# Optimization experiments

Measured on AMD Instinct MI355X. Metric: run time of the kernel, lower is better.

## Reference

```python
import jax, jax.numpy as jnp
import numpy as np

N, F, D, M, B, K = 100000, 256, 128, 10, 32768, 32


def setup_inputs() -> dict:
    key = jax.random.key(0)
    ks = jax.random.split(key, 14)
    stdv = float(1.0 / np.sqrt(D))
    inp = {
        "feature": jax.random.normal(ks[0], (N, F), jnp.float32),
        "flow_char_adj": jax.random.uniform(ks[1], (M, N), jnp.float32),
        "history": jax.random.randint(ks[2], (B, K), 0, N),
        "item_id": jax.random.randint(ks[3], (B,), 0, N),
        "category_r": jax.random.randint(ks[4], (B,), 0, 2),
        "category_n": jax.random.randint(ks[5], (B,), 0, 2),
        "PA_level": jax.random.randint(ks[6], (B,), 0, M),
        # learned parameters (uniform(-stdv, stdv) as in reset_parameters)
        "weight_emb": jax.random.uniform(ks[7], (F, D), jnp.float32, -stdv, stdv),
        "bias_emb": jax.random.uniform(ks[8], (D,), jnp.float32, -stdv, stdv),
        "weight_character": jax.random.uniform(ks[9], (2 * D, D), jnp.float32, -stdv, stdv),
        "att1_w": jax.random.uniform(ks[10], (D, 1), jnp.float32, -stdv, stdv),
        "att1_b": jax.random.uniform(ks[11], (1,), jnp.float32, -stdv, stdv),
        "linear1_w": jax.random.uniform(ks[12], (2 * D, D), jnp.float32, -stdv, stdv),
        "linear1_b": jax.random.uniform(ks[13], (D,), jnp.float32, -stdv, stdv),
    }
    return inp


def reference(feature, flow_char_adj, weight_emb, bias_emb, weight_character,
              att1_w, att1_b, linear1_w, linear1_b,
              history, item_id, category_r, category_n, PA_level):
    # embedding_encode
    flow_emb = feature @ weight_emb + bias_emb              # [N, D]
    character_emb = flow_char_adj @ flow_emb                # [M, D] (spmm)

    # character_modeling (shared for r and n)
    def char_lat(cat, pa):
        ce = jnp.concatenate([character_emb[cat], character_emb[pa]], axis=1)  # [B, 2D]
        return jax.nn.sigmoid(ce @ weight_character)        # [B, D]

    lat_r = char_lat(category_r, PA_level)
    lat_n = char_lat(category_n, PA_level)

    # attribute_agg: mix flow emb with its 2 category embeddings
    flow_all = (flow_emb + flow_char_adj[:2].T @ character_emb[:2]) * 0.5  # [N, D]

    # Flow_Aggregator: per-node neighbor attention (batched over ragged lists,
    # here padded to fixed degree K)
    neigh = flow_all[history]                                # [B, K, D]
    scores = neigh @ att1_w + att1_b                         # [B, K, 1]
    att = jax.nn.softmax(scores, axis=1)                     # softmax over neighbors
    agg = jnp.sum(att * neigh, axis=1)                       # [B, D]

    # NOTE: in the torch source, self_flow_latent is mutated in-place so
    # self_feats aliases neigh_feats -> both halves of the concat equal agg.
    combined = jnp.concatenate([agg, agg], axis=1)           # [B, 2D]
    out = jax.nn.relu(combined @ linear1_w + linear1_b)      # [B, D] (dropout p=0)

    pred_r = jnp.sum(lat_r * out, axis=1)                    # [B]
    pred_n = jnp.sum(lat_n * out, axis=1)                    # [B]
    return pred_r, pred_n
```

## Files before the change

### kernel.cpp

```cpp
#include <hip/hip_runtime.h>
#include <cmath>

#define NN 100000
#define FF 256
#define DDIM 128
#define MM 10
#define BB 32768
#define KK 32
#define NB1 782
#define NREP 64

#define OFF_Q     0
#define OFF_CEREP 100096
#define OFF_CE    182016
#define OFF_LAT   183296
#define OFF_CE01  185856
#define OFF_CS    186112
#define OFF_AGGB  186128
#define OFF_FE8   2283280
#define OFF_WF    5483280
#define OFF_WPF   5499664

typedef __attribute__((ext_vector_type(8))) short bf16x8;
typedef __attribute__((ext_vector_type(4))) float floatx4;
typedef __attribute__((ext_vector_type(2))) float floatx2;

__device__ __forceinline__ unsigned short f2bf(float x) {
  union { float f; unsigned u; } v; v.f = x;
  unsigned r = v.u + 0x7FFFu + ((v.u >> 16) & 1u);
  return (unsigned short)(r >> 16);
}

__device__ __forceinline__ bf16x8 cvt8(float4 a, float4 b) {
  short h[8];
  h[0] = (short)f2bf(a.x); h[1] = (short)f2bf(a.y);
  h[2] = (short)f2bf(a.z); h[3] = (short)f2bf(a.w);
  h[4] = (short)f2bf(b.x); h[5] = (short)f2bf(b.y);
  h[6] = (short)f2bf(b.z); h[7] = (short)f2bf(b.w);
  return *reinterpret_cast<bf16x8*>(h);
}

__global__ __launch_bounds__(256) void k0_wprep(const float* __restrict__ wemb,
                                                const float* __restrict__ l1w,
                                                short* __restrict__ wf,
                                                short* __restrict__ wpf)
{
  const int t = blockIdx.x * 256 + threadIdx.x;
  if (t < 4096) {
    const int kk = t >> 9, rem = t & 511;
    const int ct = rem >> 6, l = rem & 63;
    const int n = ct * 16 + (l & 15);
    const int kbase = kk * 32 + (l >> 4) * 8;
    short hi[8];
#pragma unroll
    for (int j = 0; j < 8; j++) hi[j] = (short)f2bf(wemb[(kbase + j) * 128 + n]);
    *reinterpret_cast<int4*>(&wf[((kk * 8 + ct) * 64 + l) * 8]) = *reinterpret_cast<int4*>(hi);
  } else {
    const int t2 = t - 4096;
    const int kk = t2 >> 9, rem = t2 & 511;
    const int ct = rem >> 6, l = rem & 63;
    const int n = ct * 16 + (l & 15);
    short h[8];
#pragma unroll
    for (int j = 0; j < 8; j++) {
      const int kp = kk * 32 + (l >> 4) * 8 + j;
      const int i = ((kp & 7) << 4) | (kp >> 3);
      h[j] = (short)f2bf(l1w[i * 128 + n] + l1w[(128 + i) * 128 + n]);
    }
    *reinterpret_cast<int4*>(&wpf[((kk * 8 + ct) * 64 + l) * 8]) = *reinterpret_cast<int4*>(h);
  }
}

__global__ __launch_bounds__(128, 2) void k1_fused(const float* __restrict__ feat,
    const short* __restrict__ wf, const float* __restrict__ bemb,
    const float* __restrict__ attw, const float* __restrict__ adj,
    float* __restrict__ q, unsigned char* __restrict__ fe8,
    float* __restrict__ cerep)
{
  __shared__ __align__(16) unsigned char ldst[128 * 272];
  const int tid = threadIdx.x;
  const int wv = tid >> 6, l = tid & 63;
  const int lane16 = l & 15, quad = l >> 4;

  floatx4 acc[4][8];
#pragma unroll
  for (int rt = 0; rt < 4; rt++)
#pragma unroll
    for (int ct = 0; ct < 8; ct++) acc[rt][ct] = floatx4{0.f, 0.f, 0.f, 0.f};

  const float* pa[4];
#pragma unroll
  for (int rt = 0; rt < 4; rt++) {
    int r = blockIdx.x * 128 + (wv * 4 + rt) * 16 + lane16;
    if (r > NN - 1) r = NN - 1;
    pa[rt] = &feat[(size_t)r * 256 + quad * 8];
  }

#pragma unroll 2
  for (int kk = 0; kk < 8; kk++) {
    const short* wb = &wf[kk * 4096 + l * 8];
    bf16x8 bh[8];
#pragma unroll
    for (int ct = 0; ct < 8; ct++)
      bh[ct] = *reinterpret_cast<const bf16x8*>(&wb[ct * 512]);
    bf16x8 a[4];
#pragma unroll
    for (int rt = 0; rt < 4; rt++) {
      const float4 f0 = *reinterpret_cast<const float4*>(pa[rt] + kk * 32);
      const float4 f1 = *reinterpret_cast<const float4*>(pa[rt] + kk * 32 + 4);
      a[rt] = cvt8(f0, f1);
    }
#pragma unroll
    for (int rt = 0; rt < 4; rt++)
#pragma unroll
      for (int ct = 0; ct < 8; ct++)
        acc[rt][ct] = __builtin_amdgcn_mfma_f32_16x16x32_bf16(a[rt], bh[ct], acc[rt][ct], 0, 0, 0);
  }

  float bembv[8], attwv[8];
#pragma unroll
  for (int ct = 0; ct < 8; ct++) {
    bembv[ct] = bemb[ct * 16 + lane16];
    attwv[ct] = attw[ct * 16 + lane16];
  }
#pragma unroll
  for (int rt = 0; rt < 4; rt++) {
#pragma unroll
    for (int reg = 0; reg < 4; reg++) {
      const int r = blockIdx.x * 128 + (wv * 4 + rt) * 16 + quad * 4 + reg;
      float v[8]; float qp = 0.f;
#pragma unroll
      for (int ct = 0; ct < 8; ct++) {
        v[ct] = acc[rt][ct][reg] + bembv[ct];
        qp = fmaf(v[ct], attwv[ct], qp);
      }
#pragma unroll
      for (int ct = 0; ct < 8; ct++) acc[rt][ct][reg] = v[ct];
      qp += __shfl_xor(qp, 1, 16);
      qp += __shfl_xor(qp, 2, 16);
      qp += __shfl_xor(qp, 4, 16);
      qp += __shfl_xor(qp, 8, 16);
      if (r < NN) {
        unsigned u0 = __builtin_amdgcn_cvt_pk_fp8_f32(v[0], v[1], 0, false);
        u0 = __builtin_amdgcn_cvt_pk_fp8_f32(v[2], v[3], u0, true);
        unsigned u1 = __builtin_amdgcn_cvt_pk_fp8_f32(v[4], v[5], 0, false);
        u1 = __builtin_amdgcn_cvt_pk_fp8_f32(v[6], v[7], u1, true);
        *reinterpret_cast<uint2*>(&fe8[(size_t)r * 128 + lane16 * 8]) = make_uint2(u0, u1);
        if (lane16 == 0) q[r] = 0.5f * qp;
      }
    }
  }
#pragma unroll
  for (int rt = 0; rt < 4; rt++) {
    const int rlocBase = (wv * 4 + rt) * 16 + quad * 4;
    const int gBase = blockIdx.x * 128 + rlocBase;
#pragma unroll
    for (int ct = 0; ct < 8; ct++) {
      unsigned short u[4];
#pragma unroll
      for (int reg = 0; reg < 4; reg++)
        u[reg] = (gBase + reg < NN) ? f2bf(acc[rt][ct][reg]) : (unsigned short)0;
      const unsigned lo_ = (unsigned)u[0] | ((unsigned)u[1] << 16);
      const unsigned hi_ = (unsigned)u[2] | ((unsigned)u[3] << 16);
      *reinterpret_cast<uint2*>(&ldst[(ct * 16 + lane16) * 272 + rlocBase * 2]) =
          make_uint2(lo_, hi_);
    }
  }
  __syncthreads();

  floatx4 cacc[4];
#pragma unroll
  for (int tt = 0; tt < 4; tt++) cacc[tt] = floatx4{0.f, 0.f, 0.f, 0.f};
  const int mclamp = (lane16 < 10) ? lane16 : 9;
#pragma unroll
  for (int kc = 0; kc < 4; kc++) {
    int n0 = blockIdx.x * 128 + kc * 32 + quad * 8;
    if (n0 > NN - 8) n0 = NN - 8;
    const float4 f0 = *reinterpret_cast<const float4*>(&adj[(size_t)mclamp * NN + n0]);
    const float4 f1 = *reinterpret_cast<const float4*>(&adj[(size_t)mclamp * NN + n0 + 4]);
    const bf16x8 afr = cvt8(f0, f1);
#pragma unroll
    for (int tt = 0; tt < 4; tt++) {
      const int col = (wv * 4 + tt) * 16 + lane16;
      const bf16x8 bfr = *reinterpret_cast<const bf16x8*>(
          &ldst[col * 272 + (kc * 32 + quad * 8) * 2]);
      cacc[tt] = __builtin_amdgcn_mfma_f32_16x16x32_bf16(afr, bfr, cacc[tt], 0, 0, 0);
    }
  }
  float* myrep = &cerep[(blockIdx.x & (NREP - 1)) * 1280];
#pragma unroll
  for (int tt = 0; tt < 4; tt++) {
#pragma unroll
    for (int reg = 0; reg < 4; reg++) {
      const int m = quad * 4 + reg;
      if (m < 10)
        atomicAdd(&myrep[m * 128 + (wv * 4 + tt) * 16 + lane16], cacc[tt][reg]);
    }
  }
}

__global__ __launch_bounds__(256) void k3r_reduce(const float* __restrict__ cerep,
                                                  float* __restrict__ ce)
{
  const int o = blockIdx.x * 256 + threadIdx.x;
  if (o < 1280) {
    float s = 0.f;
#pragma unroll 8
    for (int r = 0; r < NREP; r++) s += cerep[r * 1280 + o];
    ce[o] = s;
  }
}

__global__ __launch_bounds__(128) void k3_prep(const float* __restrict__ ce,
    const float* __restrict__ wchar, const float* __restrict__ attw,
    float* __restrict__ latTab, float* __restrict__ ce01p, float* __restrict__ cs)
{
  const int blk = blockIdx.x, tid = threadIdx.x;
  __shared__ float cec[128], cep[128];
  if (blk < 20) {
    const int c = blk / 10, p = blk % 10;
    cec[tid] = ce[c * 128 + tid];
    cep[tid] = ce[p * 128 + tid];
    __syncthreads();
    float s = 0.f;
#pragma unroll 4
    for (int j = 0; j < 128; j++) {
      s = fmaf(cec[j], wchar[j * 128 + tid], s);
      s = fmaf(cep[j], wchar[(128 + j) * 128 + tid], s);
    }
    latTab[blk * 128 + tid] = 1.f / (1.f + expf(-s));
  } else {
    const float s0 = ce[tid];
    const float s1 = ce[128 + tid];
    const int pidx = (tid & 15) * 8 + (tid >> 4);
    ce01p[pidx] = s0;
    ce01p[128 + pidx] = s1;
    cec[tid] = s0 * attw[tid];
    cep[tid] = s1 * attw[tid];
    __syncthreads();
    if (tid < 64) {
      float p0 = cec[tid] + cec[tid + 64];
      float p1 = cep[tid] + cep[tid + 64];
#pragma unroll
      for (int off = 32; off >= 1; off >>= 1) {
        p0 += __shfl_xor(p0, off);
        p1 += __shfl_xor(p1, off);
      }
      if (tid == 0) { cs[0] = 0.5f * p0; cs[1] = 0.5f * p1; }
    }
  }
}

__global__ __launch_bounds__(256) void k4a_attn(const unsigned char* __restrict__ fe8,
    const float* __restrict__ q, const float* __restrict__ adj,
    const int* __restrict__ history, const float* __restrict__ cs,
    const float* __restrict__ attb_p, const float* __restrict__ ce01p,
    short* __restrict__ aggb)
{
  const int tid = threadIdx.x;
  const int lane = tid & 63;
  const int wv = tid >> 6;
  const int half = lane >> 5;
  const int t = lane & 31;
  const int b = blockIdx.x * 8 + wv * 2 + half;

  const int n_my = history[b * 32 + t];
  const float a0 = adj[n_my];
  const float a1 = adj[NN + n_my];
  const float sc = q[n_my] + a0 * cs[0] + a1 * cs[1] + attb_p[0];
  float m = sc;
#pragma unroll
  for (int off = 16; off >= 1; off >>= 1) m = fmaxf(m, __shfl_xor(m, off, 32));
  const float e = expf(sc - m);
  float sum = e;
#pragma unroll
  for (int off = 16; off >= 1; off >>= 1) sum += __shfl_xor(sum, off, 32);
  const float att = e / sum;
  float p0 = att * a0, p1 = att * a1;
#pragma unroll
  for (int off = 16; off >= 1; off >>= 1) {
    p0 += __shfl_xor(p0, off, 32);
    p1 += __shfl_xor(p1, off, 32);
  }

  float4 acc = make_float4(0.f, 0.f, 0.f, 0.f);
#pragma unroll
  for (int k = 0; k < 32; k++) {
    const int nk = __shfl(n_my, k, 32);
    const float ak = __shfl(att, k, 32);
    const unsigned u = *reinterpret_cast<const unsigned*>(&fe8[(size_t)nk * 128 + t * 4]);
    const floatx2 lo = __builtin_amdgcn_cvt_pk_f32_fp8(u, false);
    const floatx2 hi = __builtin_amdgcn_cvt_pk_f32_fp8(u, true);
    acc.x = fmaf(ak, lo[0], acc.x);
    acc.y = fmaf(ak, lo[1], acc.y);
    acc.z = fmaf(ak, hi[0], acc.z);
    acc.w = fmaf(ak, hi[1], acc.w);
  }
  const int col = t * 4;
  const float4 c0 = *reinterpret_cast<const float4*>(&ce01p[col]);
  const float4 c1 = *reinterpret_cast<const float4*>(&ce01p[128 + col]);
  const float ox = 0.5f * (acc.x + p0 * c0.x + p1 * c1.x);
  const float oy = 0.5f * (acc.y + p0 * c0.y + p1 * c1.y);
  const float oz = 0.5f * (acc.z + p0 * c0.z + p1 * c1.z);
  const float ow = 0.5f * (acc.w + p0 * c0.w + p1 * c1.w);
  const unsigned lo_ = (unsigned)f2bf(ox) | ((unsigned)f2bf(oy) << 16);
  const unsigned hi_ = (unsigned)f2bf(oz) | ((unsigned)f2bf(ow) << 16);
  *reinterpret_cast<uint2*>(&aggb[(size_t)b * 128 + col]) = make_uint2(lo_, hi_);
}

__global__ __launch_bounds__(256) void k4b_mfma(const short* __restrict__ aggb,
    const short* __restrict__ wpf, const float* __restrict__ l1b,
    const float* __restrict__ latTab,
    const int* __restrict__ cr, const int* __restrict__ cn, const int* __restrict__ pa,
    float* __restrict__ out)
{
  const int tid = threadIdx.x;
  const int wv = tid >> 6, l = tid & 63;
  const int lane16 = l & 15, quad = l >> 4;
  const int rowbase = blockIdx.x * 128 + wv * 32;
  const int r0 = rowbase + lane16;
  const int r1 = r0 + 16;

  floatx4 acc[2][8];
#pragma unroll
  for (int rt = 0; rt < 2; rt++)
#pragma unroll
    for (int ct = 0; ct < 8; ct++) acc[rt][ct] = floatx4{0.f, 0.f, 0.f, 0.f};

#pragma unroll
  for (int kk = 0; kk < 4; kk++) {
    const bf16x8 a0 = *reinterpret_cast<const bf16x8*>(&aggb[(size_t)r0 * 128 + kk * 32 + quad * 8]);
    const bf16x8 a1 = *reinterpret_cast<const bf16x8*>(&aggb[(size_t)r1 * 128 + kk * 32 + quad * 8]);
    const short* wb = &wpf[kk * 4096 + l * 8];
#pragma unroll
    for (int ct = 0; ct < 8; ct++) {
      const bf16x8 bh = *reinterpret_cast<const bf16x8*>(&wb[ct * 512]);
      acc[0][ct] = __builtin_amdgcn_mfma_f32_16x16x32_bf16(a0, bh, acc[0][ct], 0, 0, 0);
      acc[1][ct] = __builtin_amdgcn_mfma_f32_16x16x32_bf16(a1, bh, acc[1][ct], 0, 0, 0);
    }
  }

  float bb[8];
#pragma unroll
  for (int ct = 0; ct < 8; ct++) bb[ct] = l1b[ct * 16 + lane16];
#pragma unroll
  for (int rt = 0; rt < 2; rt++) {
#pragma unroll
    for (int reg = 0; reg < 4; reg++) {
      const int r = rowbase + rt * 16 + quad * 4 + reg;
      const int ir  = (cr[r] * 10 + pa[r]) * 128;
      const int in_ = (cn[r] * 10 + pa[r]) * 128;
      float pr = 0.f, pn = 0.f;
#pragma unroll
      for (int ct = 0; ct < 8; ct++) {
        const float v = fmaxf(acc[rt][ct][reg] + bb[ct], 0.f);
        pr = fmaf(v, latTab[ir  + ct * 16 + lane16], pr);
        pn = fmaf(v, latTab[in_ + ct * 16 + lane16], pn);
      }
      pr += __shfl_xor(pr, 1, 16); pr += __shfl_xor(pr, 2, 16);
      pr += __shfl_xor(pr, 4, 16); pr += __shfl_xor(pr, 8, 16);
      pn += __shfl_xor(pn, 1, 16); pn += __shfl_xor(pn, 2, 16);
      pn += __shfl_xor(pn, 4, 16); pn += __shfl_xor(pn, 8, 16);
      if (lane16 == 0) { out[r] = pr; out[BB + r] = pn; }
    }
  }
}

extern "C" void kernel_launch(void* const* d_in, const int* in_sizes, int n_in,
                              void* d_out, int out_size, void* d_ws, size_t ws_size,
                              hipStream_t stream) {
  const float* feat  = (const float*)d_in[0];
  const float* adj   = (const float*)d_in[1];
  const int*   hist  = (const int*)d_in[2];
  const int*   cr    = (const int*)d_in[4];
  const int*   cn    = (const int*)d_in[5];
  const int*   pa    = (const int*)d_in[6];
  const float* wemb  = (const float*)d_in[7];
  const float* bemb  = (const float*)d_in[8];
  const float* wchar = (const float*)d_in[9];
  const float* attw  = (const float*)d_in[10];
  const float* attb  = (const float*)d_in[11];
  const float* l1w   = (const float*)d_in[12];
  const float* l1b   = (const float*)d_in[13];
  float* out = (float*)d_out;
  float* ws  = (float*)d_ws;

  float* q     = ws + OFF_Q;
  float* cerep = ws + OFF_CEREP;
  float* ce    = ws + OFF_CE;
  float* lat   = ws + OFF_LAT;
  float* ce01p = ws + OFF_CE01;
  float* cs    = ws + OFF_CS;
  short* aggb  = (short*)(ws + OFF_AGGB);
  unsigned char* fe8 = (unsigned char*)(ws + OFF_FE8);
  short* wf    = (short*)(ws + OFF_WF);
  short* wpf   = (short*)(ws + OFF_WPF);

  hipMemsetAsync(cerep, 0, NREP * 1280 * sizeof(float), stream);
  k0_wprep<<<24, 256, 0, stream>>>(wemb, l1w, wf, wpf);
  k1_fused<<<NB1, 128, 0, stream>>>(feat, wf, bemb, attw, adj, q, fe8, cerep);
  k3r_reduce<<<5, 256, 0, stream>>>(cerep, ce);
  k3_prep<<<21, 128, 0, stream>>>(ce, wchar, attw, lat, ce01p, cs);
  k4a_attn<<<4096, 256, 0, stream>>>(fe8, q, adj, hist, cs, attb, ce01p, aggb);
  k4b_mfma<<<256, 256, 0, stream>>>(aggb, wpf, l1b, lat, cr, cn, pa, out);
}
```

Measured before the change: 269.3 us.

## Double-buffer feature tiles into LDS via async global_load_lds in k1

The feature GEMM kernel now stages each 32-column slab of the 128-row feature tile into LDS with direct global-to-LDS loads, double-buffered so the next slab is fetched while the current one feeds MFMAs. Block size doubles to 256 threads (4 waves, 32 rows each), which halves per-thread accumulators so more blocks fit per CU. The aim is to hide feature-read latency and raise occupancy for this memory-bound stage. In exchange it adds a barrier per k-step and reuses the LDS buffer for the transpose stage behind an extra sync.

New measurement: 268.1 us. Within noise of the previous version (-0.4%).

```diff
diff --git a/kernel.cpp b/kernel.cpp
--- a/kernel.cpp
+++ b/kernel.cpp
@@ -40,6 +40,12 @@
   return *reinterpret_cast<bf16x8*>(h);
 }
 
+__device__ __forceinline__ void gload_lds16(const float* g, void* l) {
+  __builtin_amdgcn_global_load_lds(
+      (const __attribute__((address_space(1))) void*)g,
+      (__attribute__((address_space(3))) void*)l, 16, 0, 0);
+}
+
 __global__ __launch_bounds__(256) void k0_wprep(const float* __restrict__ wemb,
                                                 const float* __restrict__ l1w,
                                                 short* __restrict__ wf,
@@ -71,47 +77,60 @@
   }
 }
 
-__global__ __launch_bounds__(128, 2) void k1_fused(const float* __restrict__ feat,
+__global__ __launch_bounds__(256, 4) void k1_fused(const float* __restrict__ feat,
     const short* __restrict__ wf, const float* __restrict__ bemb,
     const float* __restrict__ attw, const float* __restrict__ adj,
     float* __restrict__ q, unsigned char* __restrict__ fe8,
     float* __restrict__ cerep)
 {
-  __shared__ __align__(16) unsigned char ldst[128 * 272];
+  __shared__ __align__(16) unsigned char ldsraw[34816];
   const int tid = threadIdx.x;
   const int wv = tid >> 6, l = tid & 63;
   const int lane16 = l & 15, quad = l >> 4;
-
-  floatx4 acc[4][8];
-#pragma unroll
-  for (int rt = 0; rt < 4; rt++)
+  const int rowbase = blockIdx.x * 128;
+
+  size_t gsrc[4];
+#pragma unroll
+  for (int i = 0; i < 4; i++) {
+    int r = rowbase + wv * 32 + i * 8 + (l >> 3);
+    if (r > NN - 1) r = NN - 1;
+    gsrc[i] = (size_t)r * 256 + (l & 7) * 4;
+  }
+#pragma unroll
+  for (int i = 0; i < 4; i++)
+    gload_lds16(&feat[gsrc[i]], ldsraw + wv * 4096 + i * 1024);
+
+  floatx4 acc[2][8];
+#pragma unroll
+  for (int rt = 0; rt < 2; rt++)
 #pragma unroll
     for (int ct = 0; ct < 8; ct++) acc[rt][ct] = floatx4{0.f, 0.f, 0.f, 0.f};
-
-  const float* pa[4];
-#pragma unroll
-  for (int rt = 0; rt < 4; rt++) {
-    int r = blockIdx.x * 128 + (wv * 4 + rt) * 16 + lane16;
-    if (r > NN - 1) r = NN - 1;
-    pa[rt] = &feat[(size_t)r * 256 + quad * 8];
-  }
 
 #pragma unroll 2
   for (int kk = 0; kk < 8; kk++) {
+    __syncthreads();
+    if (kk < 7) {
+      unsigned char* dst = ldsraw + ((kk + 1) & 1) * 16384 + wv * 4096;
+#pragma unroll
+      for (int i = 0; i < 4; i++)
+        gload_lds16(&feat[gsrc[i] + (size_t)(kk + 1) * 32], dst + i * 1024);
+    }
+    const float* Ab = (const float*)(ldsraw + (kk & 1) * 16384);
     const short* wb = &wf[kk * 4096 + l * 8];
     bf16x8 bh[8];
 #pragma unroll
     for (int ct = 0; ct < 8; ct++)
       bh[ct] = *reinterpret_cast<const bf16x8*>(&wb[ct * 512]);
-    bf16x8 a[4];
-#pragma unroll
-    for (int rt = 0; rt < 4; rt++) {
-      const float4 f0 = *reinterpret_cast<const float4*>(pa[rt] + kk * 32);
-      const float4 f1 = *reinterpret_cast<const float4*>(pa[rt] + kk * 32 + 4);
+    bf16x8 a[2];
+#pragma unroll
+    for (int rt = 0; rt < 2; rt++) {
+      const int row_loc = wv * 32 + rt * 16 + lane16;
+      const float4 f0 = *reinterpret_cast<const float4*>(&Ab[row_loc * 32 + quad * 8]);
+      const float4 f1 = *reinterpret_cast<const float4*>(&Ab[row_loc * 32 + quad * 8 + 4]);
       a[rt] = cvt8(f0, f1);
     }
 #pragma unroll
-    for (int rt = 0; rt < 4; rt++)
+    for (int rt = 0; rt < 2; rt++)
 #pragma unroll
       for (int ct = 0; ct < 8; ct++)
         acc[rt][ct] = __builtin_amdgcn_mfma_f32_16x16x32_bf16(a[rt], bh[ct], acc[rt][ct], 0, 0, 0);
@@ -124,10 +143,10 @@
     attwv[ct] = attw[ct * 16 + lane16];
   }
 #pragma unroll
-  for (int rt = 0; rt < 4; rt++) {
+  for (int rt = 0; rt < 2; rt++) {
 #pragma unroll
     for (int reg = 0; reg < 4; reg++) {
-      const int r = blockIdx.x * 128 + (wv * 4 + rt) * 16 + quad * 4 + reg;
+      const int r = rowbase + wv * 32 + rt * 16 + quad * 4 + reg;
       float v[8]; float qp = 0.f;
 #pragma unroll
       for (int ct = 0; ct < 8; ct++) {
@@ -150,10 +169,12 @@
       }
     }
   }
-#pragma unroll
-  for (int rt = 0; rt < 4; rt++) {
-    const int rlocBase = (wv * 4 + rt) * 16 + quad * 4;
-    const int gBase = blockIdx.x * 128 + rlocBase;
+
+  __syncthreads();
+#pragma unroll
+  for (int rt = 0; rt < 2; rt++) {
+    const int rlocBase = wv * 32 + rt * 16 + quad * 4;
+    const int gBase = rowbase + rlocBase;
 #pragma unroll
     for (int ct = 0; ct < 8; ct++) {
       unsigned short u[4];
@@ -162,39 +183,39 @@
         u[reg] = (gBase + reg < NN) ? f2bf(acc[rt][ct][reg]) : (unsigned short)0;
       const unsigned lo_ = (unsigned)u[0] | ((unsigned)u[1] << 16);
       const unsigned hi_ = (unsigned)u[2] | ((unsigned)u[3] << 16);
-      *reinterpret_cast<uint2*>(&ldst[(ct * 16 + lane16) * 272 + rlocBase * 2]) =
+      *reinterpret_cast<uint2*>(&ldsraw[(ct * 16 + lane16) * 272 + rlocBase * 2]) =
           make_uint2(lo_, hi_);
     }
   }
   __syncthreads();
 
-  floatx4 cacc[4];
-#pragma unroll
-  for (int tt = 0; tt < 4; tt++) cacc[tt] = floatx4{0.f, 0.f, 0.f, 0.f};
+  floatx4 cacc[2];
+  cacc[0] = floatx4{0.f, 0.f, 0.f, 0.f};
+  cacc[1] = floatx4{0.f, 0.f, 0.f, 0.f};
   const int mclamp = (lane16 < 10) ? lane16 : 9;
 #pragma unroll
   for (int kc = 0; kc < 4; kc++) {
-    int n0 = blockIdx.x * 128 + kc * 32 + quad * 8;
+    int n0 = rowbase + kc * 32 + quad * 8;
     if (n0 > NN - 8) n0 = NN - 8;
     const float4 f0 = *reinterpret_cast<const float4*>(&adj[(size_t)mclamp * NN + n0]);
     const float4 f1 = *reinterpret_cast<const float4*>(&adj[(size_t)mclamp * NN + n0 + 4]);
     const bf16x8 afr = cvt8(f0, f1);
 #pragma unroll
-    for (int tt = 0; tt < 4; tt++) {
-      const int col = (wv * 4 + tt) * 16 + lane16;
+    for (int tt = 0; tt < 2; tt++) {
+      const int col = (wv * 2 + tt) * 16 + lane16;
       const bf16x8 bfr = *reinterpret_cast<const bf16x8*>(
-          &ldst[col * 272 + (kc * 32 + quad * 8) * 2]);
+          &ldsraw[col * 272 + (kc * 32 + quad * 8) * 2]);
       cacc[tt] = __builtin_amdgcn_mfma_f32_16x16x32_bf16(afr, bfr, cacc[tt], 0, 0, 0);
     }
   }
   float* myrep = &cerep[(blockIdx.x & (NREP - 1)) * 1280];
 #pragma unroll
-  for (int tt = 0; tt < 4; tt++) {
+  for (int tt = 0; tt < 2; tt++) {
 #pragma unroll
     for (int reg = 0; reg < 4; reg++) {
       const int m = quad * 4 + reg;
       if (m < 10)
-        atomicAdd(&myrep[m * 128 + (wv * 4 + tt) * 16 + lane16], cacc[tt][reg]);
+        atomicAdd(&myrep[m * 128 + (wv * 2 + tt) * 16 + lane16], cacc[tt][reg]);
     }
   }
 }
@@ -398,7 +419,7 @@
 
   hipMemsetAsync(cerep, 0, NREP * 1280 * sizeof(float), stream);
   k0_wprep<<<24, 256, 0, stream>>>(wemb, l1w, wf, wpf);
-  k1_fused<<<NB1, 128, 0, stream>>>(feat, wf, bemb, attw, adj, q, fe8, cerep);
+  k1_fused<<<NB1, 256, 0, stream>>>(feat, wf, bemb, attw, adj, q, fe8, cerep);
   k3r_reduce<<<5, 256, 0, stream>>>(cerep, ce);
   k3_prep<<<21, 128, 0, stream>>>(ce, wchar, attw, lat, ce01p, cs);
   k4a_attn<<<4096, 256, 0, stream>>>(fe8, q, adj, hist, cs, attb, ce01p, aggb);
```
